# Performance work log

Measured on AMD Instinct MI355X. Metric: run time of the kernel, lower is better.

## Reference

```python
import jax, jax.numpy as jnp
import numpy as np

BLANK = 6735
NUM_CLASSES = 6736
LOSS_WEIGHT = 1.0
NEG = -1e30  # log-space -inf surrogate


def setup_inputs() -> dict:
    key = jax.random.key(0)
    k1, k2 = jax.random.split(key)
    N, T, C, S = 64, 64, NUM_CLASSES, 16
    pred = jax.random.normal(k1, (N, T, C), dtype=jnp.float32)
    gt = jax.random.randint(k2, (N, S), 0, BLANK, dtype=jnp.int32)  # all < blank => full target lengths
    return {"pred": pred, "gt": gt}


def _ctc_loss_mean(log_probs, targets):
    # log_probs: [N, T, C] (already log_softmax), targets: [N, S] all valid (< blank)
    N, T, C = log_probs.shape
    S = targets.shape[1]
    L = 2 * S + 1  # extended label sequence: blank-interleaved

    ext = jnp.full((N, L), BLANK, dtype=jnp.int32)
    ext = ext.at[:, 1::2].set(targets)

    # gather per-extended-label log probs: [N, T, L]
    idx = jnp.broadcast_to(ext[:, None, :], (N, T, L))
    lp_ext = jnp.take_along_axis(log_probs, idx, axis=2)

    # skip-transition allowed when label is non-blank and differs from label two back
    ext_m2 = jnp.pad(ext, ((0, 0), (2, 0)), constant_values=-1)[:, :L]
    allow2 = (ext != BLANK) & (ext != ext_m2)  # [N, L]

    alpha0 = jnp.full((N, L), NEG, dtype=log_probs.dtype)
    alpha0 = alpha0.at[:, 0].set(lp_ext[:, 0, 0])
    alpha0 = alpha0.at[:, 1].set(lp_ext[:, 0, 1])

    def step(alpha, lp_t):
        a1 = jnp.pad(alpha, ((0, 0), (1, 0)), constant_values=NEG)[:, :L]
        a2 = jnp.pad(alpha, ((0, 0), (2, 0)), constant_values=NEG)[:, :L]
        a2 = jnp.where(allow2, a2, NEG)
        m = jnp.maximum(jnp.maximum(alpha, a1), a2)
        lse = m + jnp.log(jnp.exp(alpha - m) + jnp.exp(a1 - m) + jnp.exp(a2 - m))
        return lse + lp_t, None

    alpha_T, _ = jax.lax.scan(step, alpha0, jnp.swapaxes(lp_ext, 0, 1)[1:])  # scan over t=1..T-1
    log_p = jnp.logaddexp(alpha_T[:, L - 1], alpha_T[:, L - 2])  # [N]
    nll = -log_p
    # torch CTCLoss reduction='mean': mean over batch of nll / target_length
    return jnp.mean(nll / S)


def reference(pred, gt):
    # pred: [N, T, C] logits; gt: [N, S] labels (all < blank)
    log_probs = jax.nn.log_softmax(pred, axis=2)
    return _ctc_loss_mean(log_probs, gt.astype(jnp.int32)) * LOSS_WEIGHT
```

## Files before the change

### kernel.cpp

```cpp
#include <hip/hip_runtime.h>

#define BLANK 6735
#define NEG   (-1e30f)

constexpr int Nn = 64, Tt = 64, Cc = 6736, Ss = 16, Ll = 2 * Ss + 1;
constexpr float LOG2E = 1.44269504088896340736f;
constexpr float LN2   = 0.69314718055994530942f;

__global__ __launch_bounds__(256) void logz_gather_kernel(const float* __restrict__ pred,
                                                          const int* __restrict__ gt,
                                                          float* __restrict__ lpe,
                                                          float* __restrict__ out) {
    const int row = blockIdx.x;
    const int n   = row >> 6;
    const float* prow = pred + (size_t)row * Cc;
    const float4* p = reinterpret_cast<const float4*>(prow);

    float s = 0.f;
    for (int i = threadIdx.x; i < Cc / 4; i += 256) {
        float4 v = p[i];
        s += exp2f(v.x * LOG2E) + exp2f(v.y * LOG2E) +
             exp2f(v.z * LOG2E) + exp2f(v.w * LOG2E);
    }
    for (int off = 1; off < 64; off <<= 1) s += __shfl_xor(s, off);

    __shared__ float ssum[4];
    __shared__ float slz;
    if ((threadIdx.x & 63) == 0) ssum[threadIdx.x >> 6] = s;
    __syncthreads();
    if (threadIdx.x == 0) {
        float S = ssum[0] + ssum[1] + ssum[2] + ssum[3];
        slz = __log2f(S) * LN2;
        if (row == 0) out[0] = 0.f;
    }
    __syncthreads();

    if (threadIdx.x < Ll) {
        const int l = threadIdx.x;
        const int ext = (l & 1) ? gt[n * Ss + (l >> 1)] : BLANK;
        lpe[(size_t)row * Ll + l] = prow[ext] - slz;
    }
}

__global__ __launch_bounds__(64) void ctc_kernel(const float* __restrict__ lpe,
                                                 const int* __restrict__ gt,
                                                 float* __restrict__ out) {
    const int n = blockIdx.x;
    const int l = threadIdx.x;
    const bool active = (l < Ll);

    int ext = BLANK;
    if (active && (l & 1)) ext = gt[n * Ss + (l >> 1)];
    const int ext_m2 = __shfl_up(ext, 2);
    const bool allow2 = active && (l >= 2) && (ext != BLANK) && (ext != ext_m2);

    const float* lrow = lpe + (size_t)n * Tt * Ll;

    float lp    = active ? lrow[l] : NEG;
    float alpha = (l <= 1) ? lp : NEG;

    for (int t = 1; t < Tt; ++t) {
        lp = active ? lrow[t * Ll + l] : NEG;
        float a1 = __shfl_up(alpha, 1); if (l < 1) a1 = NEG;
        float a2 = __shfl_up(alpha, 2); if (!allow2) a2 = NEG;
        float m   = fmaxf(alpha, fmaxf(a1, a2));
        float lse = m + LN2 * __log2f(exp2f((alpha - m) * LOG2E) +
                                      exp2f((a1 - m) * LOG2E) +
                                      exp2f((a2 - m) * LOG2E));
        alpha = lse + lp;
    }

    const float aL1 = __shfl(alpha, Ll - 1);
    const float aL2 = __shfl(alpha, Ll - 2);
    if (l == 0) {
        float m    = fmaxf(aL1, aL2);
        float logp = m + LN2 * __log2f(exp2f((aL1 - m) * LOG2E) +
                                       exp2f((aL2 - m) * LOG2E));
        atomicAdd(out, -logp * (1.0f / (Ss * Nn)));
    }
}

extern "C" void kernel_launch(void* const* d_in, const int* in_sizes, int n_in,
                              void* d_out, int out_size, void* d_ws, size_t ws_size,
                              hipStream_t stream) {
    const float* pred = (const float*)d_in[0];
    const int*   gt   = (const int*)d_in[1];
    float* lpe = (float*)d_ws;
    float* out = (float*)d_out;

    logz_gather_kernel<<<Nn * Tt, 256, 0, stream>>>(pred, gt, lpe, out);
    ctc_kernel<<<Nn, 64, 0, stream>>>(lpe, gt, out);
}
```

Measured before the change: 176.0 us.

## Assign one row per wavefront in logsumexp gather and unroll CTC time loop

Each 256-thread block now handles four rows, one per 64-lane wavefront, so the row reduction needs only wavefront shuffles and no shared memory or block barriers. The class loop has a fixed trip count with a predicated tail, which allows unrolling and more loads in flight. The CTC recurrence loop over time is also fully unrolled. The trade-off is fewer blocks in the grid and more serial work per wavefront.

```diff
diff --git a/kernel.cpp b/kernel.cpp
--- a/kernel.cpp
+++ b/kernel.cpp
@@ -11,35 +11,35 @@
                                                           const int* __restrict__ gt,
                                                           float* __restrict__ lpe,
                                                           float* __restrict__ out) {
-    const int row = blockIdx.x;
-    const int n   = row >> 6;
+    const int wid  = threadIdx.x >> 6;
+    const int lane = threadIdx.x & 63;
+    const int row  = (blockIdx.x << 2) + wid;
+    const int n    = row >> 6;
+
     const float* prow = pred + (size_t)row * Cc;
-    const float4* p = reinterpret_cast<const float4*>(prow);
+    const float4* p   = reinterpret_cast<const float4*>(prow);
 
     float s = 0.f;
-    for (int i = threadIdx.x; i < Cc / 4; i += 256) {
+    int i = lane;
+    for (int it = 0; it < 26; ++it, i += 64) {
         float4 v = p[i];
-        s += exp2f(v.x * LOG2E) + exp2f(v.y * LOG2E) +
-             exp2f(v.z * LOG2E) + exp2f(v.w * LOG2E);
+        s += (exp2f(v.x * LOG2E) + exp2f(v.y * LOG2E)) +
+             (exp2f(v.z * LOG2E) + exp2f(v.w * LOG2E));
+    }
+    if (lane < 20) {
+        float4 v = p[i];
+        s += (exp2f(v.x * LOG2E) + exp2f(v.y * LOG2E)) +
+             (exp2f(v.z * LOG2E) + exp2f(v.w * LOG2E));
     }
     for (int off = 1; off < 64; off <<= 1) s += __shfl_xor(s, off);
 
-    __shared__ float ssum[4];
-    __shared__ float slz;
-    if ((threadIdx.x & 63) == 0) ssum[threadIdx.x >> 6] = s;
-    __syncthreads();
-    if (threadIdx.x == 0) {
-        float S = ssum[0] + ssum[1] + ssum[2] + ssum[3];
-        slz = __log2f(S) * LN2;
-        if (row == 0) out[0] = 0.f;
+    const float slz = __log2f(s) * LN2;
+
+    if (lane < Ll) {
+        const int ext = (lane & 1) ? gt[n * Ss + (lane >> 1)] : BLANK;
+        lpe[(size_t)row * Ll + lane] = prow[ext] - slz;
     }
-    __syncthreads();
-
-    if (threadIdx.x < Ll) {
-        const int l = threadIdx.x;
-        const int ext = (l & 1) ? gt[n * Ss + (l >> 1)] : BLANK;
-        lpe[(size_t)row * Ll + l] = prow[ext] - slz;
-    }
+    if (row == 0 && lane == 0) out[0] = 0.f;
 }
 
 __global__ __launch_bounds__(64) void ctc_kernel(const float* __restrict__ lpe,
@@ -59,6 +59,7 @@
     float lp    = active ? lrow[l] : NEG;
     float alpha = (l <= 1) ? lp : NEG;
 
+    #pragma unroll
     for (int t = 1; t < Tt; ++t) {
         lp = active ? lrow[t * Ll + l] : NEG;
         float a1 = __shfl_up(alpha, 1); if (l < 1) a1 = NEG;
@@ -88,6 +89,6 @@
     float* lpe = (float*)d_ws;
     float* out = (float*)d_out;
 
-    logz_gather_kernel<<<Nn * Tt, 256, 0, stream>>>(pred, gt, lpe, out);
+    logz_gather_kernel<<<(Nn * Tt) / 4, 256, 0, stream>>>(pred, gt, lpe, out);
     ctc_kernel<<<Nn, 64, 0, stream>>>(lpe, gt, out);
 }
```

Measured after the change: 174.6 us. Within noise of the previous version (-0.8%).
